# Optimization experiments

Measured on AMD Instinct MI355X. Metric: run time of the kernel, lower is better.

The kernel has to match this reference:

```python
import jax, jax.numpy as jnp
import numpy as np

L1, L2, B, D1, D2, HEADS, M = 1024, 1024, 8, 512, 1024, 16, 1024
DPH = M // HEADS  # 64


def setup_inputs() -> dict:
    key = jax.random.key(0)
    ks = jax.random.split(key, 10)
    w = lambda k, shp: jax.random.normal(k, shp, jnp.float32) * 0.02
    z = lambda n: jnp.zeros((n,), jnp.float32)
    return {
        "ctx_1": jax.random.normal(ks[0], (L1, B, D1), jnp.float32),
        "ctx_2": jax.random.normal(ks[1], (L2, B, D2), jnp.float32),
        "Wk1": w(ks[2], (M, D1)), "bk1": z(M),
        "Wv1": w(ks[3], (M, D1)), "bv1": z(M),
        "Wk2": w(ks[4], (M, D2)), "bk2": z(M),
        "Wv2": w(ks[5], (M, D2)), "bv2": z(M),
        "Wf12": w(ks[6], (M, M)), "bf12": z(M),
        "Wf21": w(ks[7], (M, M)), "bf21": z(M),
    }


def _shape_heads(x):
    # [L, B, M] -> [B, H, L, dph]
    L, Bs, _ = x.shape
    return x.reshape(L, Bs, HEADS, DPH).transpose(1, 2, 0, 3)


def _unshape(x):
    # [B, H, L, dph] -> [L, B, M]
    Bs, Hn, L, d = x.shape
    return x.transpose(2, 0, 1, 3).reshape(L, Bs, Hn * d)


def reference(ctx_1, ctx_2, Wk1, bk1, Wv1, bv1, Wk2, bk2, Wv2, bv2,
              Wf12, bf12, Wf21, bf21):
    k1 = _shape_heads(ctx_1 @ Wk1.T + bk1)  # [B,H,L1,d]
    v1 = _shape_heads(ctx_1 @ Wv1.T + bv1)  # [B,H,L1,d]
    k2 = _shape_heads(ctx_2 @ Wk2.T + bk2)  # [B,H,L2,d]
    v2 = _shape_heads(ctx_2 @ Wv2.T + bv2)  # [B,H,L2,d]

    # scores: key_2 @ key_1^T -> [B, H, L2, L1]
    scores = jnp.einsum('bhqd,bhkd->bhqk', k2, k1)

    # direction 1 -> 2: softmax over dim=2 (the L2 axis), then AV with value_1
    dist_1_to_2 = jax.nn.softmax(scores, axis=2)
    context_1_to_2 = jnp.einsum('bhqk,bhkd->bhqd', dist_1_to_2, v1)  # [B,H,L2,d]
    context_1_to_2 = _unshape(context_1_to_2) @ Wf12.T + bf12        # [L2,B,M]

    # direction 2 -> 1: softmax over dim=1 (the head axis), transpose, AV with value_2
    dist_2_to_1 = jax.nn.softmax(scores, axis=1)
    context_2_to_1 = jnp.einsum('bhqk,bhqd->bhkd', dist_2_to_1, v2)  # [B,H,L1,d]
    context_2_to_1 = _unshape(context_2_to_1) @ Wf21.T + bf21        # [L1,B,M]

    return (context_2_to_1, context_1_to_2)
```

## Files before the change

kernel.cpp:

```cpp
#include <hip/hip_runtime.h>
#include <hip/hip_bf16.h>

constexpr int LQ  = 1024;
constexpr int BN  = 8;
constexpr int D1N = 512;
constexpr int D2N = 1024;
constexpr int HN  = 16;
constexpr int MN  = 1024;
constexpr int DPH = 64;

typedef __attribute__((ext_vector_type(8)))  short bf16x8;
typedef __attribute__((ext_vector_type(2)))  float f32x2;
typedef __attribute__((ext_vector_type(4)))  float f32x4;
typedef __attribute__((ext_vector_type(16))) float f32x16;

__device__ __forceinline__ unsigned short f2bf(float f) {
  unsigned u = __float_as_uint(f);
  u += 0x7FFFu + ((u >> 16) & 1u);
  return (unsigned short)(u >> 16);
}
__device__ __forceinline__ float bf2f(unsigned short u) {
  return __uint_as_float(((unsigned)u) << 16);
}
__device__ __forceinline__ float rcpf(float x) {
  float r;
  asm("v_rcp_f32 %0, %1" : "=v"(r) : "v"(x));
  return r;
}

__device__ __forceinline__ f32x4 mfma16(bf16x8 a, bf16x8 b, f32x4 c) {
  return __builtin_amdgcn_mfma_f32_16x16x32_bf16(a, b, c, 0, 0, 0);
}
__device__ __forceinline__ f32x16 mfma32(bf16x8 a, bf16x8 b, f32x16 c) {
  return __builtin_amdgcn_mfma_f32_32x32x16_bf16(a, b, c, 0, 0, 0);
}
__device__ __forceinline__ f32x16 zero16() {
  f32x16 z;
#pragma unroll
  for (int i = 0; i < 16; ++i) z[i] = 0.f;
  return z;
}

__device__ __forceinline__ unsigned cvtpk(float lo, float hi) {
  unsigned r;
  asm("v_cvt_pk_bf16_f32 %0, %1, %2" : "=v"(r) : "v"(lo), "v"(hi));
  return r;
}

__device__ __forceinline__ void lds_barrier() {
  asm volatile("s_waitcnt lgkmcnt(0)" ::: "memory");
  __builtin_amdgcn_s_barrier();
}

__device__ __forceinline__ bf16x8 pfrag(const float* p) {
  unsigned x0 = cvtpk(p[0], p[1]), y0 = cvtpk(p[4], p[5]);
  unsigned x1 = cvtpk(p[2], p[3]), y1 = cvtpk(p[6], p[7]);
  asm volatile("v_permlane32_swap_b32 %0, %1" : "+v"(x0), "+v"(y0));
  asm volatile("v_permlane32_swap_b32 %0, %1" : "+v"(x1), "+v"(y1));
  union { unsigned u[4]; bf16x8 v; } r;
  r.u[0] = x0; r.u[1] = x1; r.u[2] = y0; r.u[3] = y1;
  return r.v;
}

__device__ __forceinline__ bf16x8 pack8(f32x4 p0, f32x4 p1) {
  bf16x8 o;
  o[0] = (short)f2bf(p0[0]); o[1] = (short)f2bf(p0[1]);
  o[2] = (short)f2bf(p0[2]); o[3] = (short)f2bf(p0[3]);
  o[4] = (short)f2bf(p1[0]); o[5] = (short)f2bf(p1[1]);
  o[6] = (short)f2bf(p1[2]); o[7] = (short)f2bf(p1[3]);
  return o;
}
__device__ __forceinline__ bf16x8 pack8q(f32x4 lo, f32x4 hi) {
  union { unsigned u[4]; bf16x8 v; } r;
  r.u[0] = cvtpk(lo[0], lo[1]); r.u[1] = cvtpk(lo[2], lo[3]);
  r.u[2] = cvtpk(hi[0], hi[1]); r.u[3] = cvtpk(hi[2], hi[3]);
  return r.v;
}

__global__ __launch_bounds__(256) void cvt_kernel(const float* __restrict__ src,
                                                  unsigned short* __restrict__ dst,
                                                  int n8) {
  int i = blockIdx.x * blockDim.x + threadIdx.x;
  if (i >= n8) return;
  const f32x4* s = (const f32x4*)src;
  f32x4 x = s[2 * i], y = s[2 * i + 1];
  ((bf16x8*)dst)[i] = pack8(x, y);
}

__global__ __launch_bounds__(256) void addcvt_kernel(const float* __restrict__ p0,
                                                     const float* __restrict__ p1,
                                                     unsigned short* __restrict__ dst,
                                                     int n8) {
  int i = blockIdx.x * blockDim.x + threadIdx.x;
  if (i >= n8) return;
  f32x4 a0 = ((const f32x4*)p0)[2 * i],     a1 = ((const f32x4*)p0)[2 * i + 1];
  f32x4 b0 = ((const f32x4*)p1)[2 * i],     b1 = ((const f32x4*)p1)[2 * i + 1];
#pragma unroll
  for (int j = 0; j < 4; ++j) { a0[j] += b0[j]; a1[j] += b1[j]; }
  ((bf16x8*)dst)[i] = pack8q(a0, a1);
}

template <int K, int MODE, bool AF32>
__device__ __forceinline__ void gemm_body(const void* __restrict__ Ap,
                                          const unsigned short* __restrict__ W,
                                          const float* __restrict__ bias,
                                          void* __restrict__ outp,
                                          int rowb, int colb) {
  __shared__ unsigned short As[128 * 40], Bs[128 * 40];
  const int tid = threadIdx.x, wave = tid >> 6, lane = tid & 63;
  const int lg = lane >> 4, lm = lane & 15;
  const int wrow = (wave >> 1) * 64, wcol = (wave & 1) * 64;
  const int sr = tid >> 1, sh = (tid & 1) * 16;
  const unsigned short* Arow = AF32 ? nullptr
      : (const unsigned short*)Ap + (size_t)(rowb + sr) * K + sh;
  const float* ArowF = AF32 ? (const float*)Ap + (size_t)(rowb + sr) * K + sh
                            : nullptr;
  const unsigned short* Wrow = W + (size_t)(colb + sr) * K + sh;

  f32x4 acc[4][4];
#pragma unroll
  for (int i = 0; i < 4; ++i)
#pragma unroll
    for (int j = 0; j < 4; ++j) acc[i][j] = (f32x4){0.f, 0.f, 0.f, 0.f};

  f32x4 fa0, fa1, fa2, fa3;
  bf16x8 a0, a1, b0, b1;
  if (AF32) {
    fa0 = *(const f32x4*)(ArowF);     fa1 = *(const f32x4*)(ArowF + 4);
    fa2 = *(const f32x4*)(ArowF + 8); fa3 = *(const f32x4*)(ArowF + 12);
  } else {
    a0 = *(const bf16x8*)(Arow);
    a1 = *(const bf16x8*)(Arow + 8);
  }
  b0 = *(const bf16x8*)(Wrow);
  b1 = *(const bf16x8*)(Wrow + 8);

  for (int kk = 0; kk < K; kk += 32) {
    lds_barrier();
    if (AF32) {
      *(bf16x8*)&As[sr * 40 + sh]     = pack8q(fa0, fa1);
      *(bf16x8*)&As[sr * 40 + sh + 8] = pack8q(fa2, fa3);
    } else {
      *(bf16x8*)&As[sr * 40 + sh] = a0;
      *(bf16x8*)&As[sr * 40 + sh + 8] = a1;
    }
    *(bf16x8*)&Bs[sr * 40 + sh] = b0;
    *(bf16x8*)&Bs[sr * 40 + sh + 8] = b1;
    const int kn = (kk + 32 < K) ? kk + 32 : 0;
    if (AF32) {
      fa0 = *(const f32x4*)(ArowF + kn);     fa1 = *(const f32x4*)(ArowF + kn + 4);
      fa2 = *(const f32x4*)(ArowF + kn + 8); fa3 = *(const f32x4*)(ArowF + kn + 12);
    } else {
      a0 = *(const bf16x8*)(Arow + kn);
      a1 = *(const bf16x8*)(Arow + kn + 8);
    }
    b0 = *(const bf16x8*)(Wrow + kn);
    b1 = *(const bf16x8*)(Wrow + kn + 8);
    lds_barrier();
    bf16x8 af[4], wf[4];
#pragma unroll
    for (int i = 0; i < 4; ++i) af[i] = *(const bf16x8*)&As[(wrow + i * 16 + lm) * 40 + lg * 8];
#pragma unroll
    for (int j = 0; j < 4; ++j) wf[j] = *(const bf16x8*)&Bs[(wcol + j * 16 + lm) * 40 + lg * 8];
#pragma unroll
    for (int i = 0; i < 4; ++i)
#pragma unroll
      for (int j = 0; j < 4; ++j) acc[i][j] = mfma16(af[i], wf[j], acc[i][j]);
  }

#pragma unroll
  for (int j = 0; j < 4; ++j) {
    int col = colb + wcol + j * 16 + lm;
    float bs = bias[col];
#pragma unroll
    for (int i = 0; i < 4; ++i) {
#pragma unroll
      for (int r = 0; r < 4; ++r) {
        int row = rowb + wrow + i * 16 + lg * 4 + r;
        float v = acc[i][j][r] + bs;
        if (MODE == 0) {
          int l = row >> 3, bb = row & 7, h = col >> 6, d = col & 63;
          ((unsigned short*)outp)[(((size_t)(bb * HN + h)) * LQ + l) * DPH + d] = f2bf(v);
        } else {
          ((float*)outp)[(size_t)row * MN + col] = v;
        }
      }
    }
  }
}

template <int K>
__global__ __launch_bounds__(256) void gemm_pair_f32_kernel(
    const float* __restrict__ A,
    const unsigned short* __restrict__ W0, const unsigned short* __restrict__ W1,
    const float* __restrict__ b0, const float* __restrict__ b1,
    void* __restrict__ o0, void* __restrict__ o1) {
  const int sel = blockIdx.x & 1;
  gemm_body<K, 0, true>(A, sel ? W1 : W0, sel ? b1 : b0, sel ? o1 : o0,
                        (blockIdx.x >> 1) * 128, blockIdx.y * 128);
}

template <int K>
__global__ __launch_bounds__(256) void gemm_dual_kernel(
    const unsigned short* __restrict__ A0, const unsigned short* __restrict__ A1,
    const unsigned short* __restrict__ W0, const unsigned short* __restrict__ W1,
    const float* __restrict__ b0, const float* __restrict__ b1,
    void* __restrict__ o0, void* __restrict__ o1) {
  const int sel = blockIdx.y >> 3;
  gemm_body<K, 2, false>(sel ? A1 : A0, sel ? W1 : W0, sel ? b1 : b0,
                         sel ? o1 : o0, blockIdx.x * 128, (blockIdx.y & 7) * 128);
}

__global__ __launch_bounds__(256) void transpose_kernel(const unsigned short* __restrict__ V,
                                                        unsigned short* __restrict__ VT,
                                                        const float* __restrict__ scale) {
  __shared__ unsigned short t[64][72];
  int bh = blockIdx.y, l0 = blockIdx.x * 64;
  int tid = threadIdx.x;
  int r = tid >> 2, c0 = (tid & 3) * 16;
  const unsigned short* src = V + ((size_t)bh * LQ + l0 + r) * DPH + c0;
  bf16x8 v0 = *(const bf16x8*)(src);
  bf16x8 v1 = *(const bf16x8*)(src + 8);
  if (scale) {
    float sc = scale[(size_t)bh * LQ + l0 + r];
#pragma unroll
    for (int j = 0; j < 8; ++j) {
      v0[j] = (short)f2bf(bf2f((unsigned short)v0[j]) * sc);
      v1[j] = (short)f2bf(bf2f((unsigned short)v1[j]) * sc);
    }
  }
  *(bf16x8*)&t[r][c0] = v0;
  *(bf16x8*)&t[r][c0 + 8] = v1;
  __syncthreads();
  int d = tid >> 2, lc = (tid & 3) * 16;
  bf16x8 o0, o1;
#pragma unroll
  for (int j = 0; j < 8; ++j) {
    o0[j] = (short)t[lc + j][d];
    o1[j] = (short)t[lc + 8 + j][d];
  }
  unsigned short* dst = VT + ((size_t)bh * DPH + d) * LQ + l0 + lc;
  *(bf16x8*)dst = o0;
  *(bf16x8*)(dst + 8) = o1;
}

__global__ __launch_bounds__(256) void col_reduce_kernel(const unsigned short* __restrict__ K1p,
                                                         const unsigned short* __restrict__ K2p,
                                                         float* __restrict__ inv_colsum) {
  int bh = blockIdx.y, kb = blockIdx.x * 128;
  int wave = threadIdx.x >> 6, lane = threadIdx.x & 63, l31 = lane & 31, sg = lane >> 5;
  int k0w = kb + wave * 32;
  const unsigned short* k1 = K1p + (size_t)bh * LQ * DPH;
  const unsigned short* k2 = K2p + (size_t)bh * LQ * DPH;
  bf16x8 bk[4];
#pragma unroll
  for (int i = 0; i < 4; ++i)
    bk[i] = *(const bf16x8*)(k1 + (size_t)(k0w + l31) * DPH + i * 16 + sg * 8);
  float tot = 0.f;
  for (int q0 = 0; q0 < LQ; q0 += 32) {
    bf16x8 aq[4];
#pragma unroll
    for (int i = 0; i < 4; ++i)
      aq[i] = *(const bf16x8*)(k2 + (size_t)(q0 + l31) * DPH + i * 16 + sg * 8);
    f32x16 cs = zero16();
#pragma unroll
    for (int i = 0; i < 4; ++i) cs = mfma32(aq[i], bk[i], cs);
#pragma unroll
    for (int r = 0; r < 16; ++r) tot += __expf(cs[r]);
  }
  tot += __shfl_xor(tot, 32);
  if (lane < 32) inv_colsum[(size_t)bh * LQ + k0w + lane] = 1.0f / tot;
}

__global__ __launch_bounds__(256) void ctx12_kernel(const unsigned short* __restrict__ K1p,
                                                    const unsigned short* __restrict__ K2p,
                                                    const unsigned short* __restrict__ V1Ts,
                                                    unsigned short* __restrict__ c12) {
  int bh = blockIdx.y, b = bh >> 4, h = bh & 15;
  int wave = threadIdx.x >> 6, lane = threadIdx.x & 63, l31 = lane & 31, sg = lane >> 5;
  int q0 = blockIdx.x * 128 + wave * 32;
  const unsigned short* k1 = K1p + (size_t)bh * LQ * DPH;
  const unsigned short* k2 = K2p + (size_t)bh * LQ * DPH;
  const unsigned short* vt = V1Ts + (size_t)bh * DPH * LQ;

  bf16x8 bq[4];
#pragma unroll
  for (int i = 0; i < 4; ++i)
    bq[i] = *(const bf16x8*)(k2 + (size_t)(q0 + l31) * DPH + i * 16 + sg * 8);

  f32x16 acc0 = zero16(), acc1 = zero16();
  for (int k0 = 0; k0 < LQ; k0 += 32) {
    bf16x8 ak[4];
#pragma unroll
    for (int i = 0; i < 4; ++i)
      ak[i] = *(const bf16x8*)(k1 + (size_t)(k0 + l31) * DPH + i * 16 + sg * 8);
    f32x16 cs = zero16();
#pragma unroll
    for (int i = 0; i < 4; ++i) cs = mfma32(ak[i], bq[i], cs);
    float p[16];
#pragma unroll
    for (int r = 0; r < 16; ++r) p[r] = __expf(cs[r]);
    bf16x8 pa0 = pfrag(p), pa1 = pfrag(p + 8);
    bf16x8 v00 = *(const bf16x8*)(vt + (size_t)l31 * LQ + k0 + sg * 8);
    bf16x8 v01 = *(const bf16x8*)(vt + (size_t)l31 * LQ + k0 + 16 + sg * 8);
    bf16x8 v10 = *(const bf16x8*)(vt + (size_t)(32 + l31) * LQ + k0 + sg * 8);
    bf16x8 v11 = *(const bf16x8*)(vt + (size_t)(32 + l31) * LQ + k0 + 16 + sg * 8);
    acc0 = mfma32(pa0, v00, acc0);
    acc0 = mfma32(pa1, v01, acc0);
    acc1 = mfma32(pa0, v10, acc1);
    acc1 = mfma32(pa1, v11, acc1);
  }
#pragma unroll
  for (int r = 0; r < 16; ++r) {
    int q = q0 + (r & 3) + 8 * (r >> 2) + 4 * sg;
    size_t base = ((size_t)q * BN + b) * MN + h * 64;
    c12[base + l31] = f2bf(acc0[r]);
    c12[base + 32 + l31] = f2bf(acc1[r]);
  }
}

__global__ __launch_bounds__(1024) void ctx21_part_kernel(const unsigned short* __restrict__ K1p,
                                                          const unsigned short* __restrict__ K2p,
                                                          const unsigned short* __restrict__ V2T,
                                                          float* __restrict__ part) {
  constexpr int SP = 34;
  constexpr int WS = 32 * SP;
  __shared__ float strip[16 * WS];
  __shared__ float tot[WS];
  const int b = blockIdx.x, kb = blockIdx.y, qh = blockIdx.z;
  const int tid = threadIdx.x, wave = tid >> 6, lane = tid & 63;
  const int l31 = lane & 31, sg = lane >> 5;
  const int h = wave, bh = b * HN + h;
  const int k0 = kb * 32;
  const unsigned short* k1 = K1p + (size_t)bh * LQ * DPH;
  const unsigned short* k2 = K2p + (size_t)bh * LQ * DPH;
  const unsigned short* vt = V2T + (size_t)bh * DPH * LQ;
  float* mystrip = &strip[wave * WS];

  const int bk_ = tid & 31, bq2 = (tid >> 5) * 2;
  const int tbeg = qh * 16, tend = tbeg + 16;

  bf16x8 bk[4];
#pragma unroll
  for (int i = 0; i < 4; ++i)
    bk[i] = *(const bf16x8*)(k1 + (size_t)(k0 + l31) * DPH + i * 16 + sg * 8);

  bf16x8 aq[4];
#pragma unroll
  for (int i = 0; i < 4; ++i)
    aq[i] = *(const bf16x8*)(k2 + (size_t)(tbeg * 32 + l31) * DPH + i * 16 + sg * 8);

  f32x16 acc0 = zero16(), acc1 = zero16();

  for (int t = tbeg; t < tend; ++t) {
    const int q0 = t * 32;
    f32x16 cs = zero16();
#pragma unroll
    for (int i = 0; i < 4; ++i) cs = mfma32(aq[i], bk[i], cs);
    const int qn = ((t + 1) & 31) * 32;
#pragma unroll
    for (int i = 0; i < 4; ++i)
      aq[i] = *(const bf16x8*)(k2 + (size_t)(qn + l31) * DPH + i * 16 + sg * 8);
    float pex[16];
#pragma unroll
    for (int r = 0; r < 16; ++r) pex[r] = __expf(cs[r]);
#pragma unroll
    for (int g = 0; g < 4; ++g) {
      int qb = g * 8 + 4 * sg;
      *(f32x2*)&mystrip[l31 * SP + qb]     = (f32x2){pex[4 * g],     pex[4 * g + 1]};
      *(f32x2*)&mystrip[l31 * SP + qb + 2] = (f32x2){pex[4 * g + 2], pex[4 * g + 3]};
    }
    bf16x8 v00 = *(const bf16x8*)(vt + (size_t)l31 * LQ + q0 + sg * 8);
    bf16x8 v01 = *(const bf16x8*)(vt + (size_t)l31 * LQ + q0 + 16 + sg * 8);
    bf16x8 v10 = *(const bf16x8*)(vt + (size_t)(32 + l31) * LQ + q0 + sg * 8);
    bf16x8 v11 = *(const bf16x8*)(vt + (size_t)(32 + l31) * LQ + q0 + 16 + sg * 8);
    lds_barrier();
    if (tid < 512) {
      int off = bk_ * SP + bq2;
      f32x2 s = *(const f32x2*)&strip[off];
#pragma unroll
      for (int w = 1; w < 16; ++w) {
        f32x2 v = *(const f32x2*)&strip[w * WS + off];
        s.x += v.x; s.y += v.y;
      }
      f32x2 rc; rc.x = rcpf(s.x); rc.y = rcpf(s.y);
      *(f32x2*)&tot[off] = rc;
    }
    lds_barrier();
    float p8a[8], p8b[8];
#pragma unroll
    for (int g = 0; g < 4; ++g) {
      int qb = g * 8 + 4 * sg;
      f32x2 t0 = *(const f32x2*)&tot[l31 * SP + qb];
      f32x2 t1 = *(const f32x2*)&tot[l31 * SP + qb + 2];
      float* dstp = (g < 2) ? &p8a[(g & 1) * 4] : &p8b[(g & 1) * 4];
      dstp[0] = pex[4 * g]     * t0.x;
      dstp[1] = pex[4 * g + 1] * t0.y;
      dstp[2] = pex[4 * g + 2] * t1.x;
      dstp[3] = pex[4 * g + 3] * t1.y;
    }
    bf16x8 pa0 = pfrag(p8a), pa1 = pfrag(p8b);
    acc0 = mfma32(pa0, v00, acc0);
    acc0 = mfma32(pa1, v01, acc0);
    acc1 = mfma32(pa0, v10, acc1);
    acc1 = mfma32(pa1, v11, acc1);
  }
  float* dst = part + (size_t)qh * (8192 * (size_t)MN);
#pragma unroll
  for (int r = 0; r < 16; ++r) {
    int k = k0 + (r & 3) + 8 * (r >> 2) + 4 * sg;
    size_t base = ((size_t)k * BN + b) * MN + h * 64;
    dst[base + l31] = acc0[r];
    dst[base + 32 + l31] = acc1[r];
  }
}

extern "C" void kernel_launch(void* const* d_in, const int* in_sizes, int n_in,
                              void* d_out, int out_size, void* d_ws, size_t ws_size,
                              hipStream_t stream) {
  const float* ctx1 = (const float*)d_in[0];
  const float* ctx2 = (const float*)d_in[1];
  const float* Wk1 = (const float*)d_in[2];  const float* bk1 = (const float*)d_in[3];
  const float* Wv1 = (const float*)d_in[4];  const float* bv1 = (const float*)d_in[5];
  const float* Wk2 = (const float*)d_in[6];  const float* bk2 = (const float*)d_in[7];
  const float* Wv2 = (const float*)d_in[8];  const float* bv2 = (const float*)d_in[9];
  const float* Wf12 = (const float*)d_in[10]; const float* bf12 = (const float*)d_in[11];
  const float* Wf21 = (const float*)d_in[12]; const float* bf21 = (const float*)d_in[13];

  char* ws = (char*)d_ws;
  size_t off = 0;
  auto alloc = [&](size_t bytes) {
    void* p = ws + off;
    off += (bytes + 255) & ~(size_t)255;
    return p;
  };
  const size_t KV_BYTES = (size_t)BN * HN * LQ * DPH * 2;

  unsigned short* wk1b = (unsigned short*)alloc((size_t)MN * D1N * 2);
  unsigned short* wv1b = (unsigned short*)alloc((size_t)MN * D1N * 2);
  unsigned short* wk2b = (unsigned short*)alloc((size_t)MN * D2N * 2);
  unsigned short* wv2b = (unsigned short*)alloc((size_t)MN * D2N * 2);
  unsigned short* wf12b = (unsigned short*)alloc((size_t)MN * MN * 2);
  unsigned short* wf21b = (unsigned short*)alloc((size_t)MN * MN * 2);
  unsigned short* K1buf = (unsigned short*)alloc(KV_BYTES);
  unsigned short* K2buf = (unsigned short*)alloc(KV_BYTES);
  unsigned short* V1T = (unsigned short*)alloc(KV_BYTES);
  unsigned short* V2T = (unsigned short*)alloc(KV_BYTES);
  float* invcs = (float*)alloc((size_t)BN * HN * LQ * 4);
  unsigned short* c12 = (unsigned short*)alloc(KV_BYTES);
  unsigned short* c21 = (unsigned short*)alloc(KV_BYTES);
  float* c21p = (float*)alloc((size_t)2 * 8192 * MN * 4);
  unsigned short* V1tmp = c12;
  unsigned short* V2tmp = c21;

  auto cvt = [&](const float* s, unsigned short* d, int n) {
    int n8 = n / 8;
    cvt_kernel<<<(n8 + 255) / 256, 256, 0, stream>>>(s, d, n8);
  };
  cvt(Wk1, wk1b, MN * D1N);
  cvt(Wv1, wv1b, MN * D1N);
  cvt(Wk2, wk2b, MN * D2N);
  cvt(Wv2, wv2b, MN * D2N);
  cvt(Wf12, wf12b, MN * MN);
  cvt(Wf21, wf21b, MN * MN);

  gemm_pair_f32_kernel<D1N><<<dim3(128, 8), 256, 0, stream>>>(
      ctx1, wk1b, wv1b, bk1, bv1, K1buf, V1tmp);
  gemm_pair_f32_kernel<D2N><<<dim3(128, 8), 256, 0, stream>>>(
      ctx2, wk2b, wv2b, bk2, bv2, K2buf, V2tmp);

  col_reduce_kernel<<<dim3(LQ / 128, BN * HN), 256, 0, stream>>>(K1buf, K2buf, invcs);
  dim3 gt(LQ / 64, BN * HN);
  transpose_kernel<<<gt, 256, 0, stream>>>(V1tmp, V1T, invcs);
  transpose_kernel<<<gt, 256, 0, stream>>>(V2tmp, V2T, nullptr);

  ctx12_kernel<<<dim3(LQ / 128, BN * HN), 256, 0, stream>>>(K1buf, K2buf, V1T, c12);
  ctx21_part_kernel<<<dim3(BN, LQ / 32, 2), 1024, 0, stream>>>(K1buf, K2buf, V2T, c21p);
  addcvt_kernel<<<(8192 * MN / 8 + 255) / 256, 256, 0, stream>>>(
      c21p, c21p + (size_t)8192 * MN, c21, 8192 * MN / 8);

  float* out0 = (float*)d_out;
  float* out1 = out0 + (size_t)LQ * BN * MN;
  gemm_dual_kernel<MN><<<dim3(64, 16), 256, 0, stream>>>(
      c21, c12, wf21b, wf12b, bf21, bf12, out0, out1);
}
```

Before: 518.3 us.

## Fuse ctx12 and ctx21 attention kernels into one block-interleaved kernel

Merges the ctx12 kernel and the split ctx21 partial kernel into a single 1024-thread kernel. Each wave computes one ctx21 head-softmax tile and one ctx12 tile in the same loop, so the ctx12 work fills the time around the LDS barriers. The two-way q split with fp32 partials and the addcvt reduction pass are removed, and ctx21 results are written directly as bf16. This saves a launch and a large fp32 round trip through memory. In exchange the grid is half the size of the old ctx21 launch and each wave carries more registers and a longer serial loop, which may lower occupancy.

```diff
diff --git a/kernel.cpp b/kernel.cpp
--- a/kernel.cpp
+++ b/kernel.cpp
@@ -85,19 +85,6 @@
   const f32x4* s = (const f32x4*)src;
   f32x4 x = s[2 * i], y = s[2 * i + 1];
   ((bf16x8*)dst)[i] = pack8(x, y);
-}
-
-__global__ __launch_bounds__(256) void addcvt_kernel(const float* __restrict__ p0,
-                                                     const float* __restrict__ p1,
-                                                     unsigned short* __restrict__ dst,
-                                                     int n8) {
-  int i = blockIdx.x * blockDim.x + threadIdx.x;
-  if (i >= n8) return;
-  f32x4 a0 = ((const f32x4*)p0)[2 * i],     a1 = ((const f32x4*)p0)[2 * i + 1];
-  f32x4 b0 = ((const f32x4*)p1)[2 * i],     b1 = ((const f32x4*)p1)[2 * i + 1];
-#pragma unroll
-  for (int j = 0; j < 4; ++j) { a0[j] += b0[j]; a1[j] += b1[j]; }
-  ((bf16x8*)dst)[i] = pack8q(a0, a1);
 }
 
 template <int K, int MODE, bool AF32>
@@ -272,108 +259,83 @@
   if (lane < 32) inv_colsum[(size_t)bh * LQ + k0w + lane] = 1.0f / tot;
 }
 
-__global__ __launch_bounds__(256) void ctx12_kernel(const unsigned short* __restrict__ K1p,
-                                                    const unsigned short* __restrict__ K2p,
-                                                    const unsigned short* __restrict__ V1Ts,
-                                                    unsigned short* __restrict__ c12) {
-  int bh = blockIdx.y, b = bh >> 4, h = bh & 15;
-  int wave = threadIdx.x >> 6, lane = threadIdx.x & 63, l31 = lane & 31, sg = lane >> 5;
-  int q0 = blockIdx.x * 128 + wave * 32;
-  const unsigned short* k1 = K1p + (size_t)bh * LQ * DPH;
-  const unsigned short* k2 = K2p + (size_t)bh * LQ * DPH;
-  const unsigned short* vt = V1Ts + (size_t)bh * DPH * LQ;
-
-  bf16x8 bq[4];
-#pragma unroll
-  for (int i = 0; i < 4; ++i)
-    bq[i] = *(const bf16x8*)(k2 + (size_t)(q0 + l31) * DPH + i * 16 + sg * 8);
-
-  f32x16 acc0 = zero16(), acc1 = zero16();
-  for (int k0 = 0; k0 < LQ; k0 += 32) {
-    bf16x8 ak[4];
-#pragma unroll
-    for (int i = 0; i < 4; ++i)
-      ak[i] = *(const bf16x8*)(k1 + (size_t)(k0 + l31) * DPH + i * 16 + sg * 8);
-    f32x16 cs = zero16();
-#pragma unroll
-    for (int i = 0; i < 4; ++i) cs = mfma32(ak[i], bq[i], cs);
-    float p[16];
-#pragma unroll
-    for (int r = 0; r < 16; ++r) p[r] = __expf(cs[r]);
-    bf16x8 pa0 = pfrag(p), pa1 = pfrag(p + 8);
-    bf16x8 v00 = *(const bf16x8*)(vt + (size_t)l31 * LQ + k0 + sg * 8);
-    bf16x8 v01 = *(const bf16x8*)(vt + (size_t)l31 * LQ + k0 + 16 + sg * 8);
-    bf16x8 v10 = *(const bf16x8*)(vt + (size_t)(32 + l31) * LQ + k0 + sg * 8);
-    bf16x8 v11 = *(const bf16x8*)(vt + (size_t)(32 + l31) * LQ + k0 + 16 + sg * 8);
-    acc0 = mfma32(pa0, v00, acc0);
-    acc0 = mfma32(pa1, v01, acc0);
-    acc1 = mfma32(pa0, v10, acc1);
-    acc1 = mfma32(pa1, v11, acc1);
-  }
-#pragma unroll
-  for (int r = 0; r < 16; ++r) {
-    int q = q0 + (r & 3) + 8 * (r >> 2) + 4 * sg;
-    size_t base = ((size_t)q * BN + b) * MN + h * 64;
-    c12[base + l31] = f2bf(acc0[r]);
-    c12[base + 32 + l31] = f2bf(acc1[r]);
-  }
-}
-
-__global__ __launch_bounds__(1024) void ctx21_part_kernel(const unsigned short* __restrict__ K1p,
-                                                          const unsigned short* __restrict__ K2p,
-                                                          const unsigned short* __restrict__ V2T,
-                                                          float* __restrict__ part) {
+__global__ __launch_bounds__(1024) void ctx_both_kernel(const unsigned short* __restrict__ K1p,
+                                                        const unsigned short* __restrict__ K2p,
+                                                        const unsigned short* __restrict__ V1Ts,
+                                                        const unsigned short* __restrict__ V2T,
+                                                        unsigned short* __restrict__ c12,
+                                                        unsigned short* __restrict__ c21) {
   constexpr int SP = 34;
   constexpr int WS = 32 * SP;
   __shared__ float strip[16 * WS];
   __shared__ float tot[WS];
-  const int b = blockIdx.x, kb = blockIdx.y, qh = blockIdx.z;
+  const int b = blockIdx.x, kb = blockIdx.y;
   const int tid = threadIdx.x, wave = tid >> 6, lane = tid & 63;
   const int l31 = lane & 31, sg = lane >> 5;
   const int h = wave, bh = b * HN + h;
   const int k0 = kb * 32;
   const unsigned short* k1 = K1p + (size_t)bh * LQ * DPH;
   const unsigned short* k2 = K2p + (size_t)bh * LQ * DPH;
-  const unsigned short* vt = V2T + (size_t)bh * DPH * LQ;
+  const unsigned short* vt2 = V2T + (size_t)bh * DPH * LQ;
   float* mystrip = &strip[wave * WS];
-
   const int bk_ = tid & 31, bq2 = (tid >> 5) * 2;
-  const int tbeg = qh * 16, tend = tbeg + 16;
-
-  bf16x8 bk[4];
-#pragma unroll
-  for (int i = 0; i < 4; ++i)
+  const int g = (b * 32 + kb) * 16 + wave;
+  const int xq = g >> 9, rem = g & 511;
+  const int bh12 = rem >> 2, w12 = rem & 3;
+  const int q12 = xq * 128 + w12 * 32;
+  const int b12 = bh12 >> 4, h12 = bh12 & 15;
+  const unsigned short* k1b = K1p + (size_t)bh12 * LQ * DPH;
+  const unsigned short* k2b = K2p + (size_t)bh12 * LQ * DPH;
+  const unsigned short* vt1 = V1Ts + (size_t)bh12 * DPH * LQ;
+
+  bf16x8 bk[4], bq[4];
+#pragma unroll
+  for (int i = 0; i < 4; ++i) {
     bk[i] = *(const bf16x8*)(k1 + (size_t)(k0 + l31) * DPH + i * 16 + sg * 8);
-
-  bf16x8 aq[4];
-#pragma unroll
-  for (int i = 0; i < 4; ++i)
-    aq[i] = *(const bf16x8*)(k2 + (size_t)(tbeg * 32 + l31) * DPH + i * 16 + sg * 8);
-
-  f32x16 acc0 = zero16(), acc1 = zero16();
-
-  for (int t = tbeg; t < tend; ++t) {
+    bq[i] = *(const bf16x8*)(k2b + (size_t)(q12 + l31) * DPH + i * 16 + sg * 8);
+  }
+
+  f32x16 a21_0 = zero16(), a21_1 = zero16();
+  f32x16 a12_0 = zero16(), a12_1 = zero16();
+
+  for (int t = 0; t < LQ / 32; ++t) {
     const int q0 = t * 32;
-    f32x16 cs = zero16();
-#pragma unroll
-    for (int i = 0; i < 4; ++i) cs = mfma32(aq[i], bk[i], cs);
-    const int qn = ((t + 1) & 31) * 32;
-#pragma unroll
-    for (int i = 0; i < 4; ++i)
-      aq[i] = *(const bf16x8*)(k2 + (size_t)(qn + l31) * DPH + i * 16 + sg * 8);
-    float pex[16];
-#pragma unroll
-    for (int r = 0; r < 16; ++r) pex[r] = __expf(cs[r]);
-#pragma unroll
-    for (int g = 0; g < 4; ++g) {
-      int qb = g * 8 + 4 * sg;
-      *(f32x2*)&mystrip[l31 * SP + qb]     = (f32x2){pex[4 * g],     pex[4 * g + 1]};
-      *(f32x2*)&mystrip[l31 * SP + qb + 2] = (f32x2){pex[4 * g + 2], pex[4 * g + 3]};
-    }
-    bf16x8 v00 = *(const bf16x8*)(vt + (size_t)l31 * LQ + q0 + sg * 8);
-    bf16x8 v01 = *(const bf16x8*)(vt + (size_t)l31 * LQ + q0 + 16 + sg * 8);
-    bf16x8 v10 = *(const bf16x8*)(vt + (size_t)(32 + l31) * LQ + q0 + sg * 8);
-    bf16x8 v11 = *(const bf16x8*)(vt + (size_t)(32 + l31) * LQ + q0 + 16 + sg * 8);
+    {
+      bf16x8 aq[4];
+#pragma unroll
+      for (int i = 0; i < 4; ++i)
+        aq[i] = *(const bf16x8*)(k2 + (size_t)(q0 + l31) * DPH + i * 16 + sg * 8);
+      f32x16 cs = zero16();
+#pragma unroll
+      for (int i = 0; i < 4; ++i) cs = mfma32(aq[i], bk[i], cs);
+#pragma unroll
+      for (int g2 = 0; g2 < 4; ++g2) {
+        int qb = g2 * 8 + 4 * sg;
+        *(f32x2*)&mystrip[l31 * SP + qb]     = (f32x2){__expf(cs[4 * g2]),     __expf(cs[4 * g2 + 1])};
+        *(f32x2*)&mystrip[l31 * SP + qb + 2] = (f32x2){__expf(cs[4 * g2 + 2]), __expf(cs[4 * g2 + 3])};
+      }
+    }
+    {
+      bf16x8 ak[4];
+#pragma unroll
+      for (int i = 0; i < 4; ++i)
+        ak[i] = *(const bf16x8*)(k1b + (size_t)(q0 + l31) * DPH + i * 16 + sg * 8);
+      f32x16 cs12 = zero16();
+#pragma unroll
+      for (int i = 0; i < 4; ++i) cs12 = mfma32(ak[i], bq[i], cs12);
+      float p[16];
+#pragma unroll
+      for (int r = 0; r < 16; ++r) p[r] = __expf(cs12[r]);
+      bf16x8 pa0 = pfrag(p), pa1 = pfrag(p + 8);
+      bf16x8 u00 = *(const bf16x8*)(vt1 + (size_t)l31 * LQ + q0 + sg * 8);
+      bf16x8 u01 = *(const bf16x8*)(vt1 + (size_t)l31 * LQ + q0 + 16 + sg * 8);
+      bf16x8 u10 = *(const bf16x8*)(vt1 + (size_t)(32 + l31) * LQ + q0 + sg * 8);
+      bf16x8 u11 = *(const bf16x8*)(vt1 + (size_t)(32 + l31) * LQ + q0 + 16 + sg * 8);
+      a12_0 = mfma32(pa0, u00, a12_0);
+      a12_0 = mfma32(pa1, u01, a12_0);
+      a12_1 = mfma32(pa0, u10, a12_1);
+      a12_1 = mfma32(pa1, u11, a12_1);
+    }
     lds_barrier();
     if (tid < 512) {
       int off = bk_ * SP + bq2;
@@ -387,31 +349,43 @@
       *(f32x2*)&tot[off] = rc;
     }
     lds_barrier();
-    float p8a[8], p8b[8];
-#pragma unroll
-    for (int g = 0; g < 4; ++g) {
-      int qb = g * 8 + 4 * sg;
-      f32x2 t0 = *(const f32x2*)&tot[l31 * SP + qb];
-      f32x2 t1 = *(const f32x2*)&tot[l31 * SP + qb + 2];
-      float* dstp = (g < 2) ? &p8a[(g & 1) * 4] : &p8b[(g & 1) * 4];
-      dstp[0] = pex[4 * g]     * t0.x;
-      dstp[1] = pex[4 * g + 1] * t0.y;
-      dstp[2] = pex[4 * g + 2] * t1.x;
-      dstp[3] = pex[4 * g + 3] * t1.y;
-    }
-    bf16x8 pa0 = pfrag(p8a), pa1 = pfrag(p8b);
-    acc0 = mfma32(pa0, v00, acc0);
-    acc0 = mfma32(pa1, v01, acc0);
-    acc1 = mfma32(pa0, v10, acc1);
-    acc1 = mfma32(pa1, v11, acc1);
-  }
-  float* dst = part + (size_t)qh * (8192 * (size_t)MN);
+    {
+      bf16x8 v00 = *(const bf16x8*)(vt2 + (size_t)l31 * LQ + q0 + sg * 8);
+      bf16x8 v01 = *(const bf16x8*)(vt2 + (size_t)l31 * LQ + q0 + 16 + sg * 8);
+      bf16x8 v10 = *(const bf16x8*)(vt2 + (size_t)(32 + l31) * LQ + q0 + sg * 8);
+      bf16x8 v11 = *(const bf16x8*)(vt2 + (size_t)(32 + l31) * LQ + q0 + 16 + sg * 8);
+      float p8a[8], p8b[8];
+#pragma unroll
+      for (int g2 = 0; g2 < 4; ++g2) {
+        int qb = g2 * 8 + 4 * sg;
+        f32x2 e0 = *(const f32x2*)&mystrip[l31 * SP + qb];
+        f32x2 e1 = *(const f32x2*)&mystrip[l31 * SP + qb + 2];
+        f32x2 i0 = *(const f32x2*)&tot[l31 * SP + qb];
+        f32x2 i1 = *(const f32x2*)&tot[l31 * SP + qb + 2];
+        float* dstp = (g2 < 2) ? &p8a[(g2 & 1) * 4] : &p8b[(g2 & 1) * 4];
+        dstp[0] = e0.x * i0.x; dstp[1] = e0.y * i0.y;
+        dstp[2] = e1.x * i1.x; dstp[3] = e1.y * i1.y;
+      }
+      bf16x8 pa0 = pfrag(p8a), pa1 = pfrag(p8b);
+      a21_0 = mfma32(pa0, v00, a21_0);
+      a21_0 = mfma32(pa1, v01, a21_0);
+      a21_1 = mfma32(pa0, v10, a21_1);
+      a21_1 = mfma32(pa1, v11, a21_1);
+    }
+  }
 #pragma unroll
   for (int r = 0; r < 16; ++r) {
     int k = k0 + (r & 3) + 8 * (r >> 2) + 4 * sg;
     size_t base = ((size_t)k * BN + b) * MN + h * 64;
-    dst[base + l31] = acc0[r];
-    dst[base + 32 + l31] = acc1[r];
+    c21[base + l31] = f2bf(a21_0[r]);
+    c21[base + 32 + l31] = f2bf(a21_1[r]);
+  }
+#pragma unroll
+  for (int r = 0; r < 16; ++r) {
+    int q = q12 + (r & 3) + 8 * (r >> 2) + 4 * sg;
+    size_t base = ((size_t)q * BN + b12) * MN + h12 * 64;
+    c12[base + l31] = f2bf(a12_0[r]);
+    c12[base + 32 + l31] = f2bf(a12_1[r]);
   }
 }
 
@@ -449,7 +423,6 @@
   float* invcs = (float*)alloc((size_t)BN * HN * LQ * 4);
   unsigned short* c12 = (unsigned short*)alloc(KV_BYTES);
   unsigned short* c21 = (unsigned short*)alloc(KV_BYTES);
-  float* c21p = (float*)alloc((size_t)2 * 8192 * MN * 4);
   unsigned short* V1tmp = c12;
   unsigned short* V2tmp = c21;
 
@@ -474,10 +447,8 @@
   transpose_kernel<<<gt, 256, 0, stream>>>(V1tmp, V1T, invcs);
   transpose_kernel<<<gt, 256, 0, stream>>>(V2tmp, V2T, nullptr);
 
-  ctx12_kernel<<<dim3(LQ / 128, BN * HN), 256, 0, stream>>>(K1buf, K2buf, V1T, c12);
-  ctx21_part_kernel<<<dim3(BN, LQ / 32, 2), 1024, 0, stream>>>(K1buf, K2buf, V2T, c21p);
-  addcvt_kernel<<<(8192 * MN / 8 + 255) / 256, 256, 0, stream>>>(
-      c21p, c21p + (size_t)8192 * MN, c21, 8192 * MN / 8);
+  ctx_both_kernel<<<dim3(BN, LQ / 32), 1024, 0, stream>>>(
+      K1buf, K2buf, V1T, V2T, c12, c21);
 
   float* out0 = (float*)d_out;
   float* out1 = out0 + (size_t)LQ * BN * MN;
```

Measured after the change: 595.6 us. 14.9% more time.

## Fuse ctx21 split-Q partials into one pass and reorder grid block mapping

Applied to the files above, without the earlier changes.

Drops the two-way split over the query axis in the ctx21 kernel, so each block loops over all of L2 and writes bf16 output directly. This removes the fp32 partial buffer and the separate add-and-convert kernel with its memory traffic. The cost is half as many blocks (256 blocks of 1024 threads), which lowers parallelism and lengthens each block's serial loop. It also swaps grid axes in the projection GEMM, col_reduce and ctx12 kernels so that consecutive blocks share the same head or weight, aiming at better cache locality.

```diff
diff --git a/kernel.cpp b/kernel.cpp
--- a/kernel.cpp
+++ b/kernel.cpp
@@ -85,19 +85,6 @@
   const f32x4* s = (const f32x4*)src;
   f32x4 x = s[2 * i], y = s[2 * i + 1];
   ((bf16x8*)dst)[i] = pack8(x, y);
-}
-
-__global__ __launch_bounds__(256) void addcvt_kernel(const float* __restrict__ p0,
-                                                     const float* __restrict__ p1,
-                                                     unsigned short* __restrict__ dst,
-                                                     int n8) {
-  int i = blockIdx.x * blockDim.x + threadIdx.x;
-  if (i >= n8) return;
-  f32x4 a0 = ((const f32x4*)p0)[2 * i],     a1 = ((const f32x4*)p0)[2 * i + 1];
-  f32x4 b0 = ((const f32x4*)p1)[2 * i],     b1 = ((const f32x4*)p1)[2 * i + 1];
-#pragma unroll
-  for (int j = 0; j < 4; ++j) { a0[j] += b0[j]; a1[j] += b1[j]; }
-  ((bf16x8*)dst)[i] = pack8q(a0, a1);
 }
 
 template <int K, int MODE, bool AF32>
@@ -195,9 +182,9 @@
     const unsigned short* __restrict__ W0, const unsigned short* __restrict__ W1,
     const float* __restrict__ b0, const float* __restrict__ b1,
     void* __restrict__ o0, void* __restrict__ o1) {
-  const int sel = blockIdx.x & 1;
+  const int sel = blockIdx.y >> 3;
   gemm_body<K, 0, true>(A, sel ? W1 : W0, sel ? b1 : b0, sel ? o1 : o0,
-                        (blockIdx.x >> 1) * 128, blockIdx.y * 128);
+                        blockIdx.x * 128, (blockIdx.y & 7) * 128);
 }
 
 template <int K>
@@ -247,7 +234,7 @@
 __global__ __launch_bounds__(256) void col_reduce_kernel(const unsigned short* __restrict__ K1p,
                                                          const unsigned short* __restrict__ K2p,
                                                          float* __restrict__ inv_colsum) {
-  int bh = blockIdx.y, kb = blockIdx.x * 128;
+  int bh = blockIdx.x, kb = blockIdx.y * 128;
   int wave = threadIdx.x >> 6, lane = threadIdx.x & 63, l31 = lane & 31, sg = lane >> 5;
   int k0w = kb + wave * 32;
   const unsigned short* k1 = K1p + (size_t)bh * LQ * DPH;
@@ -276,9 +263,9 @@
                                                     const unsigned short* __restrict__ K2p,
                                                     const unsigned short* __restrict__ V1Ts,
                                                     unsigned short* __restrict__ c12) {
-  int bh = blockIdx.y, b = bh >> 4, h = bh & 15;
+  int bh = blockIdx.x, b = bh >> 4, h = bh & 15;
   int wave = threadIdx.x >> 6, lane = threadIdx.x & 63, l31 = lane & 31, sg = lane >> 5;
-  int q0 = blockIdx.x * 128 + wave * 32;
+  int q0 = blockIdx.y * 128 + wave * 32;
   const unsigned short* k1 = K1p + (size_t)bh * LQ * DPH;
   const unsigned short* k2 = K2p + (size_t)bh * LQ * DPH;
   const unsigned short* vt = V1Ts + (size_t)bh * DPH * LQ;
@@ -319,15 +306,15 @@
   }
 }
 
-__global__ __launch_bounds__(1024) void ctx21_part_kernel(const unsigned short* __restrict__ K1p,
-                                                          const unsigned short* __restrict__ K2p,
-                                                          const unsigned short* __restrict__ V2T,
-                                                          float* __restrict__ part) {
+__global__ __launch_bounds__(1024) void ctx21_fused_kernel(const unsigned short* __restrict__ K1p,
+                                                           const unsigned short* __restrict__ K2p,
+                                                           const unsigned short* __restrict__ V2T,
+                                                           unsigned short* __restrict__ c21) {
   constexpr int SP = 34;
   constexpr int WS = 32 * SP;
   __shared__ float strip[16 * WS];
   __shared__ float tot[WS];
-  const int b = blockIdx.x, kb = blockIdx.y, qh = blockIdx.z;
+  const int b = blockIdx.x, kb = blockIdx.y;
   const int tid = threadIdx.x, wave = tid >> 6, lane = tid & 63;
   const int l31 = lane & 31, sg = lane >> 5;
   const int h = wave, bh = b * HN + h;
@@ -338,7 +325,6 @@
   float* mystrip = &strip[wave * WS];
 
   const int bk_ = tid & 31, bq2 = (tid >> 5) * 2;
-  const int tbeg = qh * 16, tend = tbeg + 16;
 
   bf16x8 bk[4];
 #pragma unroll
@@ -348,11 +334,11 @@
   bf16x8 aq[4];
 #pragma unroll
   for (int i = 0; i < 4; ++i)
-    aq[i] = *(const bf16x8*)(k2 + (size_t)(tbeg * 32 + l31) * DPH + i * 16 + sg * 8);
+    aq[i] = *(const bf16x8*)(k2 + (size_t)(l31) * DPH + i * 16 + sg * 8);
 
   f32x16 acc0 = zero16(), acc1 = zero16();
 
-  for (int t = tbeg; t < tend; ++t) {
+  for (int t = 0; t < LQ / 32; ++t) {
     const int q0 = t * 32;
     f32x16 cs = zero16();
 #pragma unroll
@@ -405,13 +391,12 @@
     acc1 = mfma32(pa0, v10, acc1);
     acc1 = mfma32(pa1, v11, acc1);
   }
-  float* dst = part + (size_t)qh * (8192 * (size_t)MN);
 #pragma unroll
   for (int r = 0; r < 16; ++r) {
     int k = k0 + (r & 3) + 8 * (r >> 2) + 4 * sg;
     size_t base = ((size_t)k * BN + b) * MN + h * 64;
-    dst[base + l31] = acc0[r];
-    dst[base + 32 + l31] = acc1[r];
+    c21[base + l31] = f2bf(acc0[r]);
+    c21[base + 32 + l31] = f2bf(acc1[r]);
   }
 }
 
@@ -449,7 +434,6 @@
   float* invcs = (float*)alloc((size_t)BN * HN * LQ * 4);
   unsigned short* c12 = (unsigned short*)alloc(KV_BYTES);
   unsigned short* c21 = (unsigned short*)alloc(KV_BYTES);
-  float* c21p = (float*)alloc((size_t)2 * 8192 * MN * 4);
   unsigned short* V1tmp = c12;
   unsigned short* V2tmp = c21;
 
@@ -464,20 +448,18 @@
   cvt(Wf12, wf12b, MN * MN);
   cvt(Wf21, wf21b, MN * MN);
 
-  gemm_pair_f32_kernel<D1N><<<dim3(128, 8), 256, 0, stream>>>(
+  gemm_pair_f32_kernel<D1N><<<dim3(64, 16), 256, 0, stream>>>(
       ctx1, wk1b, wv1b, bk1, bv1, K1buf, V1tmp);
-  gemm_pair_f32_kernel<D2N><<<dim3(128, 8), 256, 0, stream>>>(
+  gemm_pair_f32_kernel<D2N><<<dim3(64, 16), 256, 0, stream>>>(
       ctx2, wk2b, wv2b, bk2, bv2, K2buf, V2tmp);
 
-  col_reduce_kernel<<<dim3(LQ / 128, BN * HN), 256, 0, stream>>>(K1buf, K2buf, invcs);
+  col_reduce_kernel<<<dim3(BN * HN, LQ / 128), 256, 0, stream>>>(K1buf, K2buf, invcs);
   dim3 gt(LQ / 64, BN * HN);
   transpose_kernel<<<gt, 256, 0, stream>>>(V1tmp, V1T, invcs);
   transpose_kernel<<<gt, 256, 0, stream>>>(V2tmp, V2T, nullptr);
 
-  ctx12_kernel<<<dim3(LQ / 128, BN * HN), 256, 0, stream>>>(K1buf, K2buf, V1T, c12);
-  ctx21_part_kernel<<<dim3(BN, LQ / 32, 2), 1024, 0, stream>>>(K1buf, K2buf, V2T, c21p);
-  addcvt_kernel<<<(8192 * MN / 8 + 255) / 256, 256, 0, stream>>>(
-      c21p, c21p + (size_t)8192 * MN, c21, 8192 * MN / 8);
+  ctx12_kernel<<<dim3(BN * HN, LQ / 128), 256, 0, stream>>>(K1buf, K2buf, V1T, c12);
+  ctx21_fused_kernel<<<dim3(BN, LQ / 32), 1024, 0, stream>>>(K1buf, K2buf, V2T, c21);
 
   float* out0 = (float*)d_out;
   float* out1 = out0 + (size_t)LQ * BN * MN;
```

Result: faster. 476.0 us (-8.2%).
